# Kernel tuning notes

Hardware: AMD Instinct MI355X
Metric: run time of the kernel (lower is better)

The kernel has to match this reference:

```python
import jax, jax.numpy as jnp
import numpy as np

B, S, D_IN, D_OUT, H = 2, 2048, 1024, 1024, 16
DH = D_OUT // H


def setup_inputs() -> dict:
    key = jax.random.key(0)
    ks = jax.random.split(key, 6)
    sd_in = 1.0 / np.sqrt(D_IN)
    sd_out = 1.0 / np.sqrt(D_OUT)
    return {
        "x": jax.random.normal(ks[0], (B, S, D_IN), dtype=jnp.float32),
        "Wq": jax.random.uniform(ks[1], (D_IN, D_OUT), jnp.float32, -sd_in, sd_in),
        "Wk": jax.random.uniform(ks[2], (D_IN, D_OUT), jnp.float32, -sd_in, sd_in),
        "Wv": jax.random.uniform(ks[3], (D_IN, D_OUT), jnp.float32, -sd_in, sd_in),
        "Wo": jax.random.uniform(ks[4], (D_OUT, D_OUT), jnp.float32, -sd_out, sd_out),
        "bo": jax.random.uniform(ks[5], (D_OUT,), jnp.float32, -sd_out, sd_out),
    }


def reference(x, Wq, Wk, Wv, Wo, bo):
    b, n, _ = x.shape
    dh = DH
    # project and split heads: [b, n, d_out] -> [b, H, n, dh]
    def split(t):
        return t.reshape(b, n, H, dh).transpose(0, 2, 1, 3)
    q = split(x @ Wq)
    k = split(x @ Wk)
    v = split(x @ Wv)
    scores = jnp.einsum("bhqd,bhkd->bhqk", q, k)  # [b, H, n, n]
    causal = jnp.triu(jnp.ones((n, n), dtype=bool), k=1)
    scores = jnp.where(causal, -jnp.inf, scores)
    # NOTE: source scales by sqrt(num_tokens), not sqrt(d_head) — faithful.
    scale = 1.0 / (n ** 0.5)
    attn = jax.nn.softmax(scores * scale, axis=-1)
    ctx = jnp.einsum("bhqk,bhkd->bhqd", attn, v)  # [b, H, n, dh]
    ctx = ctx.transpose(0, 2, 1, 3).reshape(b, n, H * dh)
    return ctx @ Wo + bo
```

## Files before the change

### kernel.cpp

```cpp
#include <hip/hip_runtime.h>
#include <hip/hip_bf16.h>
#include <stdint.h>

#define B_   2
#define S_   2048
#define DIN  1024
#define DOUT 1024
#define H_   16
#define DH_  64

typedef __bf16 bf16_t;
typedef bf16_t bf16x8 __attribute__((ext_vector_type(8)));
typedef float  f32x4  __attribute__((ext_vector_type(4)));

static __device__ __forceinline__ void gld_lds16(const void* g, void* l) {
  __builtin_amdgcn_global_load_lds((const __attribute__((address_space(1))) void*)g,
                                   (__attribute__((address_space(3))) void*)l, 16, 0, 0);
}

static __device__ __forceinline__ unsigned short f2bf(float f) {
  __hip_bfloat16 h = __float2bfloat16(f);
  return __builtin_bit_cast(unsigned short, h);
}

static __device__ __forceinline__ float fexp2(float x) {
#if __has_builtin(__builtin_amdgcn_exp2f)
  return __builtin_amdgcn_exp2f(x);
#else
  return exp2f(x);
#endif
}

__global__ __launch_bounds__(256) void k_convert_x(const float* __restrict__ x,
                                                   unsigned short* __restrict__ xb) {
  int i = (blockIdx.x * 256 + threadIdx.x) * 4;
  float4 v = *reinterpret_cast<const float4*>(x + i);
  ushort4 o;
  o.x = f2bf(v.x); o.y = f2bf(v.y); o.z = f2bf(v.z); o.w = f2bf(v.w);
  *reinterpret_cast<ushort4*>(xb + i) = o;
}

__global__ __launch_bounds__(256) void k_transpose_w(const float* __restrict__ Wq,
                                                     const float* __restrict__ Wk,
                                                     const float* __restrict__ Wv,
                                                     const float* __restrict__ Wo,
                                                     __hip_bfloat16* __restrict__ Wt3,
                                                     __hip_bfloat16* __restrict__ Wot) {
  __shared__ float tile[32][33];
  const int z = blockIdx.z;
  const float* src = (z == 0) ? Wq : (z == 1) ? Wk : (z == 2) ? Wv : Wo;
  __hip_bfloat16* dst = (z < 3) ? (Wt3 + (size_t)z * DIN * DOUT) : Wot;
  const int n0 = blockIdx.x * 32, k0 = blockIdx.y * 32;
  const int tx = threadIdx.x, ty = threadIdx.y;
  #pragma unroll
  for (int i = ty; i < 32; i += 8)
    tile[i][tx] = src[(size_t)(k0 + i) * DOUT + n0 + tx];
  __syncthreads();
  #pragma unroll
  for (int i = ty; i < 32; i += 8)
    dst[(size_t)(n0 + i) * DIN + k0 + tx] = __float2bfloat16(tile[tx][i]);
}

template <int MODE>
__global__ __launch_bounds__(256) void k_gemm_bt(
    const __hip_bfloat16* __restrict__ A,
    const __hip_bfloat16* __restrict__ Bt,
    __hip_bfloat16* __restrict__ Qb, __hip_bfloat16* __restrict__ Kb,
    __hip_bfloat16* __restrict__ Vtb,
    float* __restrict__ Out, const float* __restrict__ bias,
    int M, int N, int K)
{
  __shared__ __align__(16) __hip_bfloat16 As[128 * 32];
  __shared__ __align__(16) __hip_bfloat16 Bs[128 * 32];
  const int tid = threadIdx.x;
  const int lane = tid & 63, wid = tid >> 6;
  const int r15 = lane & 15, g = lane >> 4;
  const int m0 = blockIdx.x * 128, n0 = blockIdx.y * 128;
  const int wr = wid >> 1, wc = wid & 1;
  f32x4 acc[4][4] = {};

  for (int kt = 0; kt < K; kt += 32) {
    #pragma unroll
    for (int i = 0; i < 2; ++i) {
      const int li = i * 256 + tid;
      const int row = li >> 2, kb = (li & 3) * 8;
      gld_lds16(A  + (size_t)(m0 + row) * K + kt + kb, (void*)(As + (size_t)(li & ~63) * 8));
      gld_lds16(Bt + (size_t)(n0 + row) * K + kt + kb, (void*)(Bs + (size_t)(li & ~63) * 8));
    }
    __syncthreads();
    bf16x8 af[4], bfr[4];
    #pragma unroll
    for (int mi = 0; mi < 4; ++mi)
      af[mi] = *reinterpret_cast<const bf16x8*>(As + (wr * 64 + mi * 16 + r15) * 32 + g * 8);
    #pragma unroll
    for (int ni = 0; ni < 4; ++ni)
      bfr[ni] = *reinterpret_cast<const bf16x8*>(Bs + (wc * 64 + ni * 16 + r15) * 32 + g * 8);
    #pragma unroll
    for (int mi = 0; mi < 4; ++mi)
      #pragma unroll
      for (int ni = 0; ni < 4; ++ni)
        acc[mi][ni] = __builtin_amdgcn_mfma_f32_16x16x32_bf16(af[mi], bfr[ni], acc[mi][ni], 0, 0, 0);
    __syncthreads();
  }

  #pragma unroll
  for (int mi = 0; mi < 4; ++mi) {
    #pragma unroll
    for (int ni = 0; ni < 4; ++ni) {
      #pragma unroll
      for (int rr = 0; rr < 4; ++rr) {
        const int m = m0 + wr * 64 + mi * 16 + g * 4 + rr;
        const int n = n0 + wc * 64 + ni * 16 + r15;
        float v = acc[mi][ni][rr];
        if (MODE == 0) {
          const int w = n >> 10, nn = n & 1023;
          const int h = nn >> 6, dh = nn & 63;
          const int b = m >> 11, s = m & 2047;
          if (w == 0) v *= 0.022097086912079608f * 1.4426950408889634f;
          const __hip_bfloat16 hv = __float2bfloat16(v);
          const size_t bh = (size_t)(b * H_ + h);
          if (w == 0)      Qb [(bh * S_ + s) * DH_ + dh] = hv;
          else if (w == 1) Kb [(bh * S_ + s) * DH_ + dh] = hv;
          else             Vtb[(bh * DH_ + dh) * S_ + s] = hv;
        } else {
          Out[(size_t)m * N + n] = v + bias[n];
        }
      }
    }
  }
}

__global__ __launch_bounds__(256) void k_attn(
    const __hip_bfloat16* __restrict__ Qb,
    const __hip_bfloat16* __restrict__ Kb,
    const __hip_bfloat16* __restrict__ Vtb,
    __hip_bfloat16* __restrict__ Ctx)
{
  __shared__ __align__(16) __hip_bfloat16 Ks[2][64 * 64];
  __shared__ __align__(16) __hip_bfloat16 Vs[2][64 * 64];
  __shared__ __align__(16) unsigned short Pl[4][16 * 64];
  const int tid = threadIdx.x, lane = tid & 63, w = tid >> 6;
  const int r15 = lane & 15, g = lane >> 4;
  const int bh = blockIdx.x;
  const int b = bh >> 4, h = bh & 15;
  const __hip_bfloat16* Qh = Qb  + (size_t)bh * S_ * DH_;
  const __hip_bfloat16* Kh = Kb  + (size_t)bh * S_ * DH_;
  const __hip_bfloat16* Vh = Vtb + (size_t)bh * DH_ * S_;
  char* PlW = (char*)&Pl[w][0];
  const int sw = (r15 & 7);

  auto stage = [&](int bufi, int t) {
    const int kv0 = t * 64;
    #pragma unroll
    for (int i = 0; i < 2; ++i) {
      const int c = i * 256 + tid;
      const int r = c >> 3;
      const int scc = (c & 7) ^ (r & 7);
      const int cbase = i * 256 + w * 64;
      gld_lds16(Kh + (size_t)(kv0 + r) * DH_ + scc * 8, (void*)(Ks[bufi] + cbase * 8));
      gld_lds16(Vh + (size_t)r * S_ + kv0 + scc * 8,    (void*)(Vs[bufi] + cbase * 8));
    }
  };

  #pragma unroll 1
  for (int ph = 0; ph < 2; ++ph) {
    const int qb = ph ? (31 - blockIdx.y) : blockIdx.y;
    const int q = qb * 64 + w * 16 + r15;

    bf16x8 qf[2];
    #pragma unroll
    for (int ks = 0; ks < 2; ++ks)
      qf[ks] = *reinterpret_cast<const bf16x8*>(Qh + (size_t)q * DH_ + ks * 32 + g * 8);

    f32x4 of[4] = {};
    float mrow = -INFINITY, lrow = 0.f;

    const int nt = qb + 1;
    stage(0, 0);
    __syncthreads();

    for (int t = 0; t < nt; ++t) {
      const int cur = t & 1;
      if (t + 1 < nt) stage(cur ^ 1, t + 1);
      const char* Kb_ = (const char*)Ks[cur];
      const char* Vb_ = (const char*)Vs[cur];
      const int kv0 = t * 64;

      f32x4 sf[4] = {};
      __builtin_amdgcn_s_setprio(1);
      #pragma unroll
      for (int ks = 0; ks < 2; ++ks)
        #pragma unroll
        for (int c = 0; c < 4; ++c) {
          bf16x8 kf = *reinterpret_cast<const bf16x8*>(
              Kb_ + (c * 16 + r15) * 128 + (((ks * 4 + g) ^ sw) * 16));
          sf[c] = __builtin_amdgcn_mfma_f32_16x16x32_bf16(kf, qf[ks], sf[c], 0, 0, 0);
        }
      __builtin_amdgcn_s_setprio(0);

      float pv[16];
      const bool diag = (t == qb);
      #pragma unroll
      for (int c = 0; c < 4; ++c)
        #pragma unroll
        for (int r = 0; r < 4; ++r) {
          const int kv = kv0 + c * 16 + g * 4 + r;
          pv[c * 4 + r] = (diag && kv > q) ? -INFINITY : sf[c][r];
        }
      float t8[8], t4[4];
      #pragma unroll
      for (int j = 0; j < 8; ++j) t8[j] = fmaxf(pv[j], pv[j + 8]);
      #pragma unroll
      for (int j = 0; j < 4; ++j) t4[j] = fmaxf(t8[j], t8[j + 4]);
      float vmax = fmaxf(fmaxf(t4[0], t4[1]), fmaxf(t4[2], t4[3]));
      vmax = fmaxf(vmax, __shfl_xor(vmax, 16, 64));
      vmax = fmaxf(vmax, __shfl_xor(vmax, 32, 64));

      if (__any(vmax > mrow + 8.f)) {
        const float mnew = fmaxf(mrow, vmax);
        const float a = fexp2(mrow - mnew);
        lrow *= a;
        #pragma unroll
        for (int d = 0; d < 4; ++d)
          #pragma unroll
          for (int r = 0; r < 4; ++r) of[d][r] *= a;
        mrow = mnew;
      }

      float pe[16];
      #pragma unroll
      for (int j = 0; j < 16; ++j) pe[j] = fexp2(pv[j] - mrow);
      #pragma unroll
      for (int c = 0; c < 4; ++c) {
        ushort4 pw;
        pw.x = f2bf(pe[c * 4 + 0]); pw.y = f2bf(pe[c * 4 + 1]);
        pw.z = f2bf(pe[c * 4 + 2]); pw.w = f2bf(pe[c * 4 + 3]);
        const int chunk = (c * 2 + (g >> 1)) ^ sw;
        *reinterpret_cast<ushort4*>(PlW + r15 * 128 + chunk * 16 + (g & 1) * 8) = pw;
      }
      float s8[8], s4[4];
      #pragma unroll
      for (int j = 0; j < 8; ++j) s8[j] = pe[j] + pe[j + 8];
      #pragma unroll
      for (int j = 0; j < 4; ++j) s4[j] = s8[j] + s8[j + 4];
      float psum = (s4[0] + s4[1]) + (s4[2] + s4[3]);
      psum += __shfl_xor(psum, 16, 64);
      psum += __shfl_xor(psum, 32, 64);
      lrow += psum;

      __builtin_amdgcn_s_setprio(1);
      #pragma unroll
      for (int ks = 0; ks < 2; ++ks) {
        bf16x8 pf = *reinterpret_cast<const bf16x8*>(
            PlW + r15 * 128 + (((ks * 4 + g) ^ sw) * 16));
        #pragma unroll
        for (int d = 0; d < 4; ++d) {
          bf16x8 vf = *reinterpret_cast<const bf16x8*>(
              Vb_ + (d * 16 + r15) * 128 + (((ks * 4 + g) ^ sw) * 16));
          of[d] = __builtin_amdgcn_mfma_f32_16x16x32_bf16(vf, pf, of[d], 0, 0, 0);
        }
      }
      __builtin_amdgcn_s_setprio(0);
      __syncthreads();
    }

    const float inv = 1.0f / lrow;
    unsigned short* Cp = (unsigned short*)Ctx + ((size_t)(b * S_ + q) * H_ + h) * DH_;
    #pragma unroll
    for (int d = 0; d < 4; ++d) {
      ushort4 ov;
      ov.x = f2bf(of[d][0] * inv); ov.y = f2bf(of[d][1] * inv);
      ov.z = f2bf(of[d][2] * inv); ov.w = f2bf(of[d][3] * inv);
      *reinterpret_cast<ushort4*>(Cp + d * 16 + g * 4) = ov;
    }
  }
}

extern "C" void kernel_launch(void* const* d_in, const int* in_sizes, int n_in,
                              void* d_out, int out_size, void* d_ws, size_t ws_size,
                              hipStream_t stream) {
  const float* x  = (const float*)d_in[0];
  const float* Wq = (const float*)d_in[1];
  const float* Wk = (const float*)d_in[2];
  const float* Wv = (const float*)d_in[3];
  const float* Wo = (const float*)d_in[4];
  const float* bo = (const float*)d_in[5];
  float* out = (float*)d_out;

  uint8_t* ws = (uint8_t*)d_ws;
  __hip_bfloat16* xb  = (__hip_bfloat16*)(ws);
  __hip_bfloat16* Wt3 = (__hip_bfloat16*)(ws + 8388608);
  __hip_bfloat16* Wot = (__hip_bfloat16*)(ws + 14680064);
  __hip_bfloat16* Qb  = (__hip_bfloat16*)(ws + 16777216);
  __hip_bfloat16* Kb  = (__hip_bfloat16*)(ws + 25165824);
  __hip_bfloat16* Vtb = (__hip_bfloat16*)(ws + 33554432);
  __hip_bfloat16* Ctx = (__hip_bfloat16*)(ws + 41943040);

  k_convert_x<<<4096, 256, 0, stream>>>(x, (unsigned short*)xb);
  k_transpose_w<<<dim3(32, 32, 4), dim3(32, 8), 0, stream>>>(Wq, Wk, Wv, Wo, Wt3, Wot);
  k_gemm_bt<0><<<dim3(32, 24), 256, 0, stream>>>(xb, Wt3, Qb, Kb, Vtb, nullptr, nullptr,
                                                 4096, 3072, 1024);
  k_attn<<<dim3(32, 16), 256, 0, stream>>>(Qb, Kb, Vtb, Ctx);
  k_gemm_bt<1><<<dim3(32, 8), 256, 0, stream>>>(Ctx, Wot, nullptr, nullptr, nullptr,
                                                out, bo, 4096, 1024, 1024);
}
```

Baseline: 129.4 us.

## Double-buffer GEMM LDS tiles, raise MFMA priority, vectorize V-transpose stores

The projection GEMM now double-buffers its A/B LDS tiles, so the async global-to-LDS load for the next K step is issued before the MFMAs on the current one, with one barrier per iteration. MFMA sections run at raised wave priority via s_setprio. The transposed V epilogue packs four consecutive sequence positions into one 8-byte store instead of four scalar stores. The cost is double the GEMM shared-memory footprint, which may lower occupancy.

After: 117.4 us. 9.3% less time.

```diff
diff --git a/kernel.cpp b/kernel.cpp
--- a/kernel.cpp
+++ b/kernel.cpp
@@ -70,8 +70,8 @@
     float* __restrict__ Out, const float* __restrict__ bias,
     int M, int N, int K)
 {
-  __shared__ __align__(16) __hip_bfloat16 As[128 * 32];
-  __shared__ __align__(16) __hip_bfloat16 Bs[128 * 32];
+  __shared__ __align__(16) __hip_bfloat16 As[2][128 * 32];
+  __shared__ __align__(16) __hip_bfloat16 Bs[2][128 * 32];
   const int tid = threadIdx.x;
   const int lane = tid & 63, wid = tid >> 6;
   const int r15 = lane & 15, g = lane >> 4;
@@ -79,52 +79,70 @@
   const int wr = wid >> 1, wc = wid & 1;
   f32x4 acc[4][4] = {};
 
-  for (int kt = 0; kt < K; kt += 32) {
+  auto stage = [&](int bi, int kt) {
     #pragma unroll
     for (int i = 0; i < 2; ++i) {
-      const int li = i * 256 + tid;
-      const int row = li >> 2, kb = (li & 3) * 8;
-      gld_lds16(A  + (size_t)(m0 + row) * K + kt + kb, (void*)(As + (size_t)(li & ~63) * 8));
-      gld_lds16(Bt + (size_t)(n0 + row) * K + kt + kb, (void*)(Bs + (size_t)(li & ~63) * 8));
-    }
-    __syncthreads();
+      const int c = i * 256 + tid;
+      const int row = c >> 2, kb = (c & 3) * 8;
+      gld_lds16(A  + (size_t)(m0 + row) * K + kt + kb, (void*)(As[bi] + (size_t)(c & ~63) * 8));
+      gld_lds16(Bt + (size_t)(n0 + row) * K + kt + kb, (void*)(Bs[bi] + (size_t)(c & ~63) * 8));
+    }
+  };
+
+  const int NT = K >> 5;
+  stage(0, 0);
+  __syncthreads();
+  int bi = 0;
+  for (int t = 0; t < NT; ++t) {
+    if (t + 1 < NT) stage(bi ^ 1, (t + 1) * 32);
     bf16x8 af[4], bfr[4];
     #pragma unroll
     for (int mi = 0; mi < 4; ++mi)
-      af[mi] = *reinterpret_cast<const bf16x8*>(As + (wr * 64 + mi * 16 + r15) * 32 + g * 8);
+      af[mi] = *reinterpret_cast<const bf16x8*>(As[bi] + (wr * 64 + mi * 16 + r15) * 32 + g * 8);
     #pragma unroll
     for (int ni = 0; ni < 4; ++ni)
-      bfr[ni] = *reinterpret_cast<const bf16x8*>(Bs + (wc * 64 + ni * 16 + r15) * 32 + g * 8);
+      bfr[ni] = *reinterpret_cast<const bf16x8*>(Bs[bi] + (wc * 64 + ni * 16 + r15) * 32 + g * 8);
+    __builtin_amdgcn_s_setprio(1);
     #pragma unroll
     for (int mi = 0; mi < 4; ++mi)
       #pragma unroll
       for (int ni = 0; ni < 4; ++ni)
         acc[mi][ni] = __builtin_amdgcn_mfma_f32_16x16x32_bf16(af[mi], bfr[ni], acc[mi][ni], 0, 0, 0);
+    __builtin_amdgcn_s_setprio(0);
     __syncthreads();
+    bi ^= 1;
   }
 
   #pragma unroll
   for (int mi = 0; mi < 4; ++mi) {
     #pragma unroll
     for (int ni = 0; ni < 4; ++ni) {
-      #pragma unroll
-      for (int rr = 0; rr < 4; ++rr) {
-        const int m = m0 + wr * 64 + mi * 16 + g * 4 + rr;
-        const int n = n0 + wc * 64 + ni * 16 + r15;
-        float v = acc[mi][ni][rr];
-        if (MODE == 0) {
-          const int w = n >> 10, nn = n & 1023;
-          const int h = nn >> 6, dh = nn & 63;
-          const int b = m >> 11, s = m & 2047;
-          if (w == 0) v *= 0.022097086912079608f * 1.4426950408889634f;
-          const __hip_bfloat16 hv = __float2bfloat16(v);
-          const size_t bh = (size_t)(b * H_ + h);
-          if (w == 0)      Qb [(bh * S_ + s) * DH_ + dh] = hv;
-          else if (w == 1) Kb [(bh * S_ + s) * DH_ + dh] = hv;
-          else             Vtb[(bh * DH_ + dh) * S_ + s] = hv;
+      const int mb = m0 + wr * 64 + mi * 16 + g * 4;
+      const int n  = n0 + wc * 64 + ni * 16 + r15;
+      if (MODE == 0) {
+        const int w = n >> 10, nn = n & 1023;
+        const int h = nn >> 6, dh = nn & 63;
+        const int b = mb >> 11, s = mb & 2047;
+        const size_t bh = (size_t)(b * H_ + h);
+        if (w == 2) {
+          ushort4 pv;
+          pv.x = f2bf(acc[mi][ni][0]); pv.y = f2bf(acc[mi][ni][1]);
+          pv.z = f2bf(acc[mi][ni][2]); pv.w = f2bf(acc[mi][ni][3]);
+          *reinterpret_cast<ushort4*>((unsigned short*)Vtb + (bh * DH_ + dh) * S_ + s) = pv;
         } else {
-          Out[(size_t)m * N + n] = v + bias[n];
+          #pragma unroll
+          for (int rr = 0; rr < 4; ++rr) {
+            float v = acc[mi][ni][rr];
+            if (w == 0) v *= 0.022097086912079608f * 1.4426950408889634f;
+            const __hip_bfloat16 hv = __float2bfloat16(v);
+            if (w == 0) Qb[(bh * S_ + s + rr) * DH_ + dh] = hv;
+            else        Kb[(bh * S_ + s + rr) * DH_ + dh] = hv;
+          }
         }
+      } else {
+        #pragma unroll
+        for (int rr = 0; rr < 4; ++rr)
+          Out[(size_t)(mb + rr) * N + n] = acc[mi][ni][rr] + bias[n];
       }
     }
   }
```
